# Kernel optimization log

Measured on AMD Instinct MI355X. Metric: run time of the kernel, lower is better.

Reference implementation:

```python
import jax, jax.numpy as jnp
import numpy as np

SIGMA = 1.0


def _sq_dists(a, b):
    # ||a_i - b_j||^2 via gemm: (n_a, n_b)
    aa = jnp.sum(a * a, axis=1)[:, None]
    bb = jnp.sum(b * b, axis=1)[None, :]
    ab = a @ b.T
    return jnp.maximum(aa + bb - 2.0 * ab, 0.0)


def _rbf(a, b, sigma):
    return jnp.exp(-_sq_dists(a, b) / (2.0 * sigma * sigma))


def setup_inputs() -> dict:
    key = jax.random.key(0)
    kx, ky = jax.random.split(key)
    x = jax.random.normal(kx, (4096, 1024), dtype=jnp.float32)
    y = jax.random.normal(ky, (4096, 1024), dtype=jnp.float32)
    return {"x": x, "y": y}


def reference(x, y):
    # Flatten non-batch dims (module accepts (n, f1, f2, ...))
    xf = x.reshape(x.shape[0], -1)
    yf = y.reshape(y.shape[0], -1)
    n = xf.shape[0]
    m = yf.shape[0]

    k_xx = _rbf(xf, xf, SIGMA)
    k_yy = _rbf(yf, yf, SIGMA)
    k_xy = _rbf(xf, yf, SIGMA)

    # Unbiased estimator: exclude diagonal of k_xx / k_yy
    sum_xx = jnp.sum(k_xx) - jnp.trace(k_xx)
    sum_yy = jnp.sum(k_yy) - jnp.trace(k_yy)
    sum_xy = jnp.sum(k_xy)

    mmd2 = (sum_xx / (n * (n - 1))
            + sum_yy / (m * (m - 1))
            - 2.0 * sum_xy / (n * m))
    return mmd2
```

## Files before the change

### kernel.cpp

```cpp
#include <hip/hip_runtime.h>


#define NROWS 4096
#define KDIM  1024
#define BM 128
#define BN 128
#define SLAB 128
#define SLABBYTES (BM * SLAB)
#define NT   32
#define TRI  528
#define NXY  1024

typedef unsigned short u16;
typedef unsigned char  u8;
typedef __attribute__((ext_vector_type(8))) int   int8v;
typedef __attribute__((ext_vector_type(4))) int   int4v;
typedef __attribute__((ext_vector_type(8))) short short8;
typedef __attribute__((ext_vector_type(4))) float f32x4;

__global__ void mmd_zero_sums(float* sums) {
    if (threadIdx.x < 3) sums[threadIdx.x] = 0.0f;
}

__device__ __forceinline__ void async_copy16(const void* g, void* l) {
    __builtin_amdgcn_global_load_lds(
        (const __attribute__((address_space(1))) unsigned int*)g,
        (__attribute__((address_space(3))) unsigned int*)l, 16, 0, 0);
}

__global__ __launch_bounds__(256) void mmd_prep8(const float* __restrict__ x,
                                                 const float* __restrict__ y,
                                                 float* __restrict__ aa,
                                                 float* __restrict__ bb,
                                                 u8* __restrict__ xb,
                                                 u8* __restrict__ yb,
                                                 float* __restrict__ sums) {
    if (blockIdx.x == 0 && blockIdx.y == 0 && threadIdx.x < 3) sums[threadIdx.x] = 0.0f;
    const int row = blockIdx.x;
    const float* src = blockIdx.y ? y : x;
    float* ndst = blockIdx.y ? bb : aa;
    u8* bdst    = blockIdx.y ? yb : xb;
    const float4 v = ((const float4*)(src + (size_t)row * KDIM))[threadIdx.x];
    int p = 0;
    p = __builtin_amdgcn_cvt_pk_fp8_f32(v.x, v.y, p, false);
    p = __builtin_amdgcn_cvt_pk_fp8_f32(v.z, v.w, p, true);
    ((int*)(bdst + (size_t)row * KDIM))[threadIdx.x] = p;
    float s = v.x * v.x + v.y * v.y + v.z * v.z + v.w * v.w;
    #pragma unroll
    for (int off = 32; off; off >>= 1) s += __shfl_down(s, off, 64);
    __shared__ float ws[4];
    if ((threadIdx.x & 63) == 0) ws[threadIdx.x >> 6] = s;
    __syncthreads();
    if (threadIdx.x == 0) ndst[row] = ws[0] + ws[1] + ws[2] + ws[3];
}

__global__ __launch_bounds__(256, 3) void mmd_tile_fp8(const u8* __restrict__ xb,
                                                       const u8* __restrict__ yb,
                                                       const float* __restrict__ aa,
                                                       const float* __restrict__ bb,
                                                       float* __restrict__ sums) {
    int mode, ti, tj;
    const int bid = blockIdx.x;
    if (bid < NXY) {
        mode = 2;
        const int st = bid >> 6;
        const int wi = bid & 63;
        ti = (st >> 2) * 8 + (wi >> 3);
        tj = (st & 3) * 8 + (wi & 7);
    } else {
        int s = bid - NXY;
        mode = (s >= TRI) ? 1 : 0;
        if (s >= TRI) s -= TRI;
        int t = (int)(32.5f - sqrtf(32.5f * 32.5f - 2.0f * (float)s));
        while (t > 0 && t * (65 - t) / 2 > s) t--;
        while ((t + 1) * (64 - t) / 2 <= s) t++;
        ti = t;
        tj = t + (s - t * (65 - t) / 2);
    }

    const u8*    __restrict__ A  = (mode == 1) ? yb : xb;
    const u8*    __restrict__ B  = (mode == 0) ? xb : yb;
    const float* __restrict__ na = (mode == 1) ? bb : aa;
    const float* __restrict__ nb = (mode == 0) ? aa : bb;

    __shared__ u8 As[SLABBYTES];
    __shared__ u8 Bs[SLABBYTES];

    const int t = threadIdx.x;
    const int w = t >> 6;
    const int l = t & 63;

    const int lrow = l >> 3;
    const int gch  = (l & 7) ^ lrow;
    const u8* aS[4]; const u8* bS[4]; int ldso[4];
    #pragma unroll
    for (int a = 0; a < 4; a++) {
        const int blk = a * 4 + w;
        const int row = blk * 8 + lrow;
        aS[a] = A + (size_t)(ti * BM + row) * KDIM + gch * 16;
        bS[a] = B + (size_t)(tj * BN + row) * KDIM + gch * 16;
        ldso[a] = blk * 1024 + l * 16;
    }

    const int wm = (w >> 1) * 64;
    const int wn = (w & 1) * 64;
    const int r  = l & 15;
    const int h  = l >> 4;
    const int s0 = (2 * h) ^ (r & 7);
    const int aB0 = (wm + r) * 128 + s0 * 16;
    const int bB0 = (wn + r) * 128 + s0 * 16;

    f32x4 acc[4][4] = {};

    for (int k0 = 0; k0 < KDIM; k0 += SLAB) {
        if (k0) __syncthreads();
        #pragma unroll
        for (int a = 0; a < 4; a++) {
            async_copy16(aS[a] + k0, &As[ldso[a]]);
            async_copy16(bS[a] + k0, &Bs[ldso[a]]);
        }
        __syncthreads();

        int8v af[4], bf[4];
        #pragma unroll
        for (int im = 0; im < 4; im++) {
            union { int8v v; int4v hh[2]; } u;
            u.hh[0] = *(const int4v*)(As + (aB0 + im * 2048));
            u.hh[1] = *(const int4v*)(As + ((aB0 + im * 2048) ^ 16));
            af[im] = u.v;
        }
        #pragma unroll
        for (int in = 0; in < 4; in++) {
            union { int8v v; int4v hh[2]; } u;
            u.hh[0] = *(const int4v*)(Bs + (bB0 + in * 2048));
            u.hh[1] = *(const int4v*)(Bs + ((bB0 + in * 2048) ^ 16));
            bf[in] = u.v;
        }
        #pragma unroll
        for (int im = 0; im < 4; im++)
            #pragma unroll
            for (int in = 0; in < 4; in++)
                acc[im][in] = __builtin_amdgcn_mfma_scale_f32_16x16x128_f8f6f4(
                    af[im], bf[in], acc[im][in],
                    0 , 0 ,
                    0, 127,
                    0, 127);
    }

    const int giBase = ti * BM + wm + h * 4;
    const int gjBase = tj * BN + wn + r;
    float nav[4][4], nbv[4];
    #pragma unroll
    for (int im = 0; im < 4; im++)
        #pragma unroll
        for (int rr = 0; rr < 4; rr++) nav[im][rr] = na[giBase + im * 16 + rr];
    #pragma unroll
    for (int in = 0; in < 4; in++) nbv[in] = nb[gjBase + in * 16];

    float lsum = 0.0f;
    #pragma unroll
    for (int im = 0; im < 4; im++) {
        #pragma unroll
        for (int in = 0; in < 4; in++) {
            const int gj = gjBase + in * 16;
            #pragma unroll
            for (int rr = 0; rr < 4; rr++) {
                const int gi = giBase + im * 16 + rr;
                float d = fmaxf(nav[im][rr] + nbv[in] - 2.0f * acc[im][in][rr], 0.0f);
                float v = __expf(-0.5f * d);
                float wgt = (mode == 2) ? 1.0f : ((gj > gi) ? 2.0f : 0.0f);
                lsum = fmaf(wgt, v, lsum);
            }
        }
    }
    #pragma unroll
    for (int off = 32; off; off >>= 1) lsum += __shfl_down(lsum, off, 64);
    __shared__ float red[4];
    if (l == 0) red[w] = lsum;
    __syncthreads();
    if (t == 0) atomicAdd(&sums[mode], red[0] + red[1] + red[2] + red[3]);
}

__device__ __forceinline__ unsigned pk_bf16(float lo, float hi) {
    unsigned ul = __float_as_uint(lo); ul += 0x7fffu + ((ul >> 16) & 1u);
    unsigned uh = __float_as_uint(hi); uh += 0x7fffu + ((uh >> 16) & 1u);
    return (ul >> 16) | (uh & 0xffff0000u);
}

__global__ __launch_bounds__(256) void mmd_row_norms(const float* __restrict__ x,
                                                     const float* __restrict__ y,
                                                     float* __restrict__ aa,
                                                     float* __restrict__ bb) {
    const int row = blockIdx.x;
    const float* src = blockIdx.y ? y : x;
    float* dst = blockIdx.y ? bb : aa;
    const float4 v = ((const float4*)(src + (size_t)row * KDIM))[threadIdx.x];
    float s = v.x * v.x + v.y * v.y + v.z * v.z + v.w * v.w;
    #pragma unroll
    for (int off = 32; off; off >>= 1) s += __shfl_down(s, off, 64);
    __shared__ float ws[4];
    if ((threadIdx.x & 63) == 0) ws[threadIdx.x >> 6] = s;
    __syncthreads();
    if (threadIdx.x == 0) dst[row] = ws[0] + ws[1] + ws[2] + ws[3];
}

#define LDST 40
#define BK 32
__global__ __launch_bounds__(256) void mmd_tile_v2(const float* __restrict__ x,
                                                   const float* __restrict__ y,
                                                   const float* __restrict__ aa,
                                                   const float* __restrict__ bb,
                                                   float* __restrict__ sums) {
    const int mode = blockIdx.z;
    const int ti = blockIdx.y, tj = blockIdx.x;
    if (mode < 2 && tj < ti) return;
    const float* __restrict__ A  = (mode == 1) ? y : x;
    const float* __restrict__ B  = (mode == 0) ? x : y;
    const float* __restrict__ na = (mode == 1) ? bb : aa;
    const float* __restrict__ nb = (mode == 0) ? aa : bb;
    __shared__ u16 As[BM * LDST];
    __shared__ u16 Bs[BN * LDST];
    const int t = threadIdx.x;
    const int srow = t >> 1;
    const int skb  = (t & 1) * 16;
    const float* aptr = A + (size_t)(ti * BM + srow) * KDIM + skb;
    const float* bptr = B + (size_t)(tj * BN + srow) * KDIM + skb;
    u16* aDst = &As[srow * LDST + skb];
    u16* bDst = &Bs[srow * LDST + skb];
    const int l  = t & 63;
    const int wv = t >> 6;
    const int wm = (wv >> 1) * 64;
    const int wn = (wv & 1) * 64;
    const int q  = l >> 4;
    const int c  = l & 15;
    const u16* aFrag = &As[(wm + c) * LDST + q * 8];
    const u16* bFrag = &Bs[(wn + c) * LDST + q * 8];
    f32x4 acc[4][4] = {};
    float4 pa[4], pb[4];
    #pragma unroll
    for (int i = 0; i < 4; i++) {
        pa[i] = *(const float4*)(aptr + i * 4);
        pb[i] = *(const float4*)(bptr + i * 4);
    }
    for (int k0 = 0; k0 < KDIM; k0 += BK) {
        uint4 w0, w1;
        w0.x = pk_bf16(pa[0].x, pa[0].y); w0.y = pk_bf16(pa[0].z, pa[0].w);
        w0.z = pk_bf16(pa[1].x, pa[1].y); w0.w = pk_bf16(pa[1].z, pa[1].w);
        w1.x = pk_bf16(pa[2].x, pa[2].y); w1.y = pk_bf16(pa[2].z, pa[2].w);
        w1.z = pk_bf16(pa[3].x, pa[3].y); w1.w = pk_bf16(pa[3].z, pa[3].w);
        __syncthreads();
        ((uint4*)aDst)[0] = w0; ((uint4*)aDst)[1] = w1;
        w0.x = pk_bf16(pb[0].x, pb[0].y); w0.y = pk_bf16(pb[0].z, pb[0].w);
        w0.z = pk_bf16(pb[1].x, pb[1].y); w0.w = pk_bf16(pb[1].z, pb[1].w);
        w1.x = pk_bf16(pb[2].x, pb[2].y); w1.y = pk_bf16(pb[2].z, pb[2].w);
        w1.z = pk_bf16(pb[3].x, pb[3].y); w1.w = pk_bf16(pb[3].z, pb[3].w);
        ((uint4*)bDst)[0] = w0; ((uint4*)bDst)[1] = w1;
        __syncthreads();
        if (k0 + BK < KDIM) {
            #pragma unroll
            for (int i = 0; i < 4; i++) {
                pa[i] = *(const float4*)(aptr + k0 + BK + i * 4);
                pb[i] = *(const float4*)(bptr + k0 + BK + i * 4);
            }
        }
        short8 af[4], bf[4];
        #pragma unroll
        for (int im = 0; im < 4; im++) af[im] = *(const short8*)(aFrag + im * 16 * LDST);
        #pragma unroll
        for (int in = 0; in < 4; in++) bf[in] = *(const short8*)(bFrag + in * 16 * LDST);
        #pragma unroll
        for (int im = 0; im < 4; im++)
            #pragma unroll
            for (int in = 0; in < 4; in++)
                acc[im][in] = __builtin_amdgcn_mfma_f32_16x16x32_bf16(af[im], bf[in], acc[im][in], 0, 0, 0);
    }
    const int giBase = ti * BM + wm + q * 4;
    const int gjBase = tj * BN + wn + c;
    float lsum = 0.0f;
    #pragma unroll
    for (int im = 0; im < 4; im++) {
        #pragma unroll
        for (int in = 0; in < 4; in++) {
            const int gj = gjBase + in * 16;
            #pragma unroll
            for (int rr = 0; rr < 4; rr++) {
                const int gi = giBase + im * 16 + rr;
                float d = fmaxf(na[gi] + nb[gj] - 2.0f * acc[im][in][rr], 0.0f);
                float v = __expf(-0.5f * d);
                float wgt = (mode == 2) ? 1.0f : ((gj > gi) ? 2.0f : 0.0f);
                lsum = fmaf(wgt, v, lsum);
            }
        }
    }
    #pragma unroll
    for (int off = 32; off; off >>= 1) lsum += __shfl_down(lsum, off, 64);
    __shared__ float red[4];
    if (l == 0) red[wv] = lsum;
    __syncthreads();
    if (t == 0) atomicAdd(&sums[mode], red[0] + red[1] + red[2] + red[3]);
}

__global__ void mmd_finalize(const float* __restrict__ sums, float* __restrict__ out, int n, int m) {
    if (threadIdx.x == 0) {
        float fn = (float)n, fm = (float)m;
        out[0] = sums[0] / (fn * (fn - 1.0f))
               + sums[1] / (fm * (fm - 1.0f))
               - 2.0f * sums[2] / (fn * fm);
    }
}

extern "C" void kernel_launch(void* const* d_in, const int* in_sizes, int n_in,
                              void* d_out, int out_size, void* d_ws, size_t ws_size,
                              hipStream_t stream) {
    const float* x = (const float*)d_in[0];
    const float* y = (const float*)d_in[1];
    float* out = (float*)d_out;

    char* ws = (char*)d_ws;
    float* aa   = (float*)(ws);
    float* bb   = (float*)(ws + 16384);
    float* sums = (float*)(ws + 32768);
    u8*    xb   = (u8*)(ws + 33024);
    u8*    yb   = xb + (size_t)NROWS * KDIM;

    const size_t needed = 33024 + 2 * (size_t)NROWS * KDIM;
    const int n = in_sizes[0] / KDIM;
    const int m = in_sizes[1] / KDIM;

    if (ws_size >= needed) {
        hipLaunchKernelGGL(mmd_prep8, dim3(NROWS, 2), dim3(256), 0, stream,
                           x, y, aa, bb, xb, yb, sums);
        hipLaunchKernelGGL(mmd_tile_fp8, dim3(NXY + 2 * TRI), dim3(256), 0, stream,
                           xb, yb, aa, bb, sums);
    } else {
        hipLaunchKernelGGL(mmd_zero_sums, dim3(1), dim3(64), 0, stream, sums);
        hipLaunchKernelGGL(mmd_row_norms, dim3(NROWS, 2), dim3(256), 0, stream, x, y, aa, bb);
        hipLaunchKernelGGL(mmd_tile_v2, dim3(NROWS / BN, NROWS / BM, 3), dim3(256), 0, stream,
                           x, y, aa, bb, sums);
    }
    hipLaunchKernelGGL(mmd_finalize, dim3(1), dim3(1), 0, stream, sums, out, n, m);
}
```

Measured before the change: 124.7 us.

## Shrink fp8 tile to 128x64, remap triangle blocks, and swizzle block order per XCD

Halves the B tile width of the fp8 MFMA kernel to 64 columns. This doubles the block count, lowers accumulator registers and LDS per block, and raises the occupancy hint from 3 to 4. The triangular index mapping is recomputed for the rectangular 32x64 tile grid of the symmetric Kxx/Kyy blocks. Block IDs are permuted with a stride of 520 so consecutive blocks land on the same XCD for L2 locality. Smaller tiles lower arithmetic intensity and increase global/L2 traffic for the A operand.

```diff
diff --git a/kernel.cpp b/kernel.cpp
--- a/kernel.cpp
+++ b/kernel.cpp
@@ -4,12 +4,15 @@
 #define NROWS 4096
 #define KDIM  1024
 #define BM 128
-#define BN 128
+#define BN 64
 #define SLAB 128
-#define SLABBYTES (BM * SLAB)
-#define NT   32
-#define TRI  528
-#define NXY  1024
+#define ASLAB (BM * SLAB)
+#define BSLAB (BN * SLAB)
+#define NTI 32
+#define NTJ 64
+#define NXY 2048
+#define TRI 1056
+#define NBLK (NXY + 2 * TRI)
 
 typedef unsigned short u16;
 typedef unsigned char  u8;
@@ -54,28 +57,31 @@
     if (threadIdx.x == 0) ndst[row] = ws[0] + ws[1] + ws[2] + ws[3];
 }
 
-__global__ __launch_bounds__(256, 3) void mmd_tile_fp8(const u8* __restrict__ xb,
+__global__ __launch_bounds__(256, 4) void mmd_tile_fp8(const u8* __restrict__ xb,
                                                        const u8* __restrict__ yb,
                                                        const float* __restrict__ aa,
                                                        const float* __restrict__ bb,
                                                        float* __restrict__ sums) {
+    const int bid = (blockIdx.x & 7) * 520 + (blockIdx.x >> 3);
+
     int mode, ti, tj;
-    const int bid = blockIdx.x;
     if (bid < NXY) {
         mode = 2;
         const int st = bid >> 6;
         const int wi = bid & 63;
-        ti = (st >> 2) * 8 + (wi >> 3);
-        tj = (st & 3) * 8 + (wi & 7);
+        ti = (st >> 3) * 8 + (wi >> 3);
+        tj = (st & 7) * 8 + (wi & 7);
     } else {
         int s = bid - NXY;
         mode = (s >= TRI) ? 1 : 0;
         if (s >= TRI) s -= TRI;
-        int t = (int)(32.5f - sqrtf(32.5f * 32.5f - 2.0f * (float)s));
-        while (t > 0 && t * (65 - t) / 2 > s) t--;
-        while ((t + 1) * (64 - t) / 2 <= s) t++;
+        int t = (int)(32.5f - sqrtf(1056.25f - (float)s));
+        if (t < 0) t = 0;
+        if (t > 31) t = 31;
+        while (t > 0 && t * (65 - t) > s) t--;
+        while (t < 31 && (t + 1) * (64 - t) <= s) t++;
         ti = t;
-        tj = t + (s - t * (65 - t) / 2);
+        tj = 2 * t + (s - t * (65 - t));
     }
 
     const u8*    __restrict__ A  = (mode == 1) ? yb : xb;
@@ -83,8 +89,9 @@
     const float* __restrict__ na = (mode == 1) ? bb : aa;
     const float* __restrict__ nb = (mode == 0) ? aa : bb;
 
-    __shared__ u8 As[SLABBYTES];
-    __shared__ u8 Bs[SLABBYTES];
+    __shared__ u8 As[ASLAB];
+    __shared__ u8 Bs[BSLAB];
+    __shared__ float red[4];
 
     const int t = threadIdx.x;
     const int w = t >> 6;
@@ -92,36 +99,39 @@
 
     const int lrow = l >> 3;
     const int gch  = (l & 7) ^ lrow;
-    const u8* aS[4]; const u8* bS[4]; int ldso[4];
+    const u8* aS[4]; const u8* bS[2]; int lA[4], lB[2];
     #pragma unroll
     for (int a = 0; a < 4; a++) {
         const int blk = a * 4 + w;
-        const int row = blk * 8 + lrow;
-        aS[a] = A + (size_t)(ti * BM + row) * KDIM + gch * 16;
-        bS[a] = B + (size_t)(tj * BN + row) * KDIM + gch * 16;
-        ldso[a] = blk * 1024 + l * 16;
+        aS[a] = A + (size_t)(ti * BM + blk * 8 + lrow) * KDIM + gch * 16;
+        lA[a] = blk * 1024 + l * 16;
+    }
+    #pragma unroll
+    for (int b = 0; b < 2; b++) {
+        const int blk = b * 4 + w;
+        bS[b] = B + (size_t)(tj * BN + blk * 8 + lrow) * KDIM + gch * 16;
+        lB[b] = blk * 1024 + l * 16;
     }
 
     const int wm = (w >> 1) * 64;
-    const int wn = (w & 1) * 64;
+    const int wn = (w & 1) * 32;
     const int r  = l & 15;
     const int h  = l >> 4;
     const int s0 = (2 * h) ^ (r & 7);
     const int aB0 = (wm + r) * 128 + s0 * 16;
     const int bB0 = (wn + r) * 128 + s0 * 16;
 
-    f32x4 acc[4][4] = {};
+    f32x4 acc[4][2] = {};
 
     for (int k0 = 0; k0 < KDIM; k0 += SLAB) {
         if (k0) __syncthreads();
         #pragma unroll
-        for (int a = 0; a < 4; a++) {
-            async_copy16(aS[a] + k0, &As[ldso[a]]);
-            async_copy16(bS[a] + k0, &Bs[ldso[a]]);
-        }
+        for (int a = 0; a < 4; a++) async_copy16(aS[a] + k0, &As[lA[a]]);
+        #pragma unroll
+        for (int b = 0; b < 2; b++) async_copy16(bS[b] + k0, &Bs[lB[b]]);
         __syncthreads();
 
-        int8v af[4], bf[4];
+        int8v af[4], bf[2];
         #pragma unroll
         for (int im = 0; im < 4; im++) {
             union { int8v v; int4v hh[2]; } u;
@@ -130,7 +140,7 @@
             af[im] = u.v;
         }
         #pragma unroll
-        for (int in = 0; in < 4; in++) {
+        for (int in = 0; in < 2; in++) {
             union { int8v v; int4v hh[2]; } u;
             u.hh[0] = *(const int4v*)(Bs + (bB0 + in * 2048));
             u.hh[1] = *(const int4v*)(Bs + ((bB0 + in * 2048) ^ 16));
@@ -139,7 +149,7 @@
         #pragma unroll
         for (int im = 0; im < 4; im++)
             #pragma unroll
-            for (int in = 0; in < 4; in++)
+            for (int in = 0; in < 2; in++)
                 acc[im][in] = __builtin_amdgcn_mfma_scale_f32_16x16x128_f8f6f4(
                     af[im], bf[in], acc[im][in],
                     0 , 0 ,
@@ -149,19 +159,19 @@
 
     const int giBase = ti * BM + wm + h * 4;
     const int gjBase = tj * BN + wn + r;
-    float nav[4][4], nbv[4];
+    float nav[4][4], nbv[2];
     #pragma unroll
     for (int im = 0; im < 4; im++)
         #pragma unroll
         for (int rr = 0; rr < 4; rr++) nav[im][rr] = na[giBase + im * 16 + rr];
     #pragma unroll
-    for (int in = 0; in < 4; in++) nbv[in] = nb[gjBase + in * 16];
+    for (int in = 0; in < 2; in++) nbv[in] = nb[gjBase + in * 16];
 
     float lsum = 0.0f;
     #pragma unroll
     for (int im = 0; im < 4; im++) {
         #pragma unroll
-        for (int in = 0; in < 4; in++) {
+        for (int in = 0; in < 2; in++) {
             const int gj = gjBase + in * 16;
             #pragma unroll
             for (int rr = 0; rr < 4; rr++) {
@@ -175,7 +185,6 @@
     }
     #pragma unroll
     for (int off = 32; off; off >>= 1) lsum += __shfl_down(lsum, off, 64);
-    __shared__ float red[4];
     if (l == 0) red[w] = lsum;
     __syncthreads();
     if (t == 0) atomicAdd(&sums[mode], red[0] + red[1] + red[2] + red[3]);
@@ -204,6 +213,7 @@
     if (threadIdx.x == 0) dst[row] = ws[0] + ws[1] + ws[2] + ws[3];
 }
 
+#define FBM 128
 #define LDST 40
 #define BK 32
 __global__ __launch_bounds__(256) void mmd_tile_v2(const float* __restrict__ x,
@@ -218,13 +228,13 @@
     const float* __restrict__ B  = (mode == 0) ? x : y;
     const float* __restrict__ na = (mode == 1) ? bb : aa;
     const float* __restrict__ nb = (mode == 0) ? aa : bb;
-    __shared__ u16 As[BM * LDST];
-    __shared__ u16 Bs[BN * LDST];
+    __shared__ u16 As[FBM * LDST];
+    __shared__ u16 Bs[FBM * LDST];
     const int t = threadIdx.x;
     const int srow = t >> 1;
     const int skb  = (t & 1) * 16;
-    const float* aptr = A + (size_t)(ti * BM + srow) * KDIM + skb;
-    const float* bptr = B + (size_t)(tj * BN + srow) * KDIM + skb;
+    const float* aptr = A + (size_t)(ti * FBM + srow) * KDIM + skb;
+    const float* bptr = B + (size_t)(tj * FBM + srow) * KDIM + skb;
     u16* aDst = &As[srow * LDST + skb];
     u16* bDst = &Bs[srow * LDST + skb];
     const int l  = t & 63;
@@ -274,8 +284,8 @@
             for (int in = 0; in < 4; in++)
                 acc[im][in] = __builtin_amdgcn_mfma_f32_16x16x32_bf16(af[im], bf[in], acc[im][in], 0, 0, 0);
     }
-    const int giBase = ti * BM + wm + q * 4;
-    const int gjBase = tj * BN + wn + c;
+    const int giBase = ti * FBM + wm + q * 4;
+    const int gjBase = tj * FBM + wn + c;
     float lsum = 0.0f;
     #pragma unroll
     for (int im = 0; im < 4; im++) {
@@ -330,12 +340,12 @@
     if (ws_size >= needed) {
         hipLaunchKernelGGL(mmd_prep8, dim3(NROWS, 2), dim3(256), 0, stream,
                            x, y, aa, bb, xb, yb, sums);
-        hipLaunchKernelGGL(mmd_tile_fp8, dim3(NXY + 2 * TRI), dim3(256), 0, stream,
+        hipLaunchKernelGGL(mmd_tile_fp8, dim3(NBLK), dim3(256), 0, stream,
                            xb, yb, aa, bb, sums);
     } else {
         hipLaunchKernelGGL(mmd_zero_sums, dim3(1), dim3(64), 0, stream, sums);
         hipLaunchKernelGGL(mmd_row_norms, dim3(NROWS, 2), dim3(256), 0, stream, x, y, aa, bb);
-        hipLaunchKernelGGL(mmd_tile_v2, dim3(NROWS / BN, NROWS / BM, 3), dim3(256), 0, stream,
+        hipLaunchKernelGGL(mmd_tile_v2, dim3(NROWS / FBM, NROWS / FBM, 3), dim3(256), 0, stream,
                            x, y, aa, bb, sums);
     }
     hipLaunchKernelGGL(mmd_finalize, dim3(1), dim3(1), 0, stream, sums, out, n, m);
```

Result: slower. 139.9 us (+12.2%).
